# Kernel tuning notes

Hardware: AMD Instinct MI355X
Metric: run time of the kernel (lower is better)

## Reference

```python
import jax, jax.numpy as jnp
import numpy as np

B, S, D = 2, 2048, 2048
H, HD = 16, 128          # n_heads, head_dim
RD = 64                  # rope_head_dim
ND = HD - RD             # nope_head_dim = 64
KVR, QR = 512, 1024      # kv_lora_rank, q_lora_rank
BASE = 10000.0
NEG = -1e30


def _apply_rope(t):
    # t: [B, H, S, RD]; GPT-NeoX half-split rotation
    half = RD // 2
    seq = t.shape[2]
    inv_freq = 1.0 / (BASE ** (jnp.arange(half, dtype=jnp.float32) / half))
    ang = jnp.arange(seq, dtype=jnp.float32)[:, None] * inv_freq  # [S, half]
    cos, sin = jnp.cos(ang), jnp.sin(ang)
    t1, t2 = t[..., :half], t[..., half:]
    return jnp.concatenate([t1 * cos - t2 * sin, t1 * sin + t2 * cos], axis=-1)


def setup_inputs() -> dict:
    key = jax.random.key(0)
    ks = jax.random.split(key, 9)
    def w(k, shape):  # weights stored [in, out], so y = x @ W
        return jax.random.normal(k, shape, jnp.float32) * (shape[0] ** -0.5)
    return {
        "x": jax.random.normal(ks[0], (B, S, D), jnp.float32),
        "Wq_down": w(ks[1], (D, QR)),
        "Wq_up": w(ks[2], (QR, H * ND)),
        "Wq_rope": w(ks[3], (QR, H * RD)),
        "Wkv_down": w(ks[4], (D, KVR)),
        "Wk_up": w(ks[5], (KVR, H * ND)),
        "Wk_rope": w(ks[6], (D, H * RD)),
        "Wv_up": w(ks[7], (KVR, H * HD)),
        "Wo": w(ks[8], (H * HD, D)),
    }


def reference(x, Wq_down, Wq_up, Wq_rope, Wkv_down, Wk_up, Wk_rope, Wv_up, Wo):
    b, s, _ = x.shape
    # low-rank query path
    q_lat = x @ Wq_down                                            # [B,S,QR]
    q_nope = (q_lat @ Wq_up).reshape(b, s, H, ND).transpose(0, 2, 1, 3)
    q_pe = (q_lat @ Wq_rope).reshape(b, s, H, RD).transpose(0, 2, 1, 3)
    # low-rank KV path (decoupled rope key comes straight from x)
    kv_lat = x @ Wkv_down                                          # [B,S,KVR]
    k_nope = (kv_lat @ Wk_up).reshape(b, s, H, ND).transpose(0, 2, 1, 3)
    k_pe = (x @ Wk_rope).reshape(b, s, H, RD).transpose(0, 2, 1, 3)
    v = (kv_lat @ Wv_up).reshape(b, s, H, HD).transpose(0, 2, 1, 3)
    # decoupled RoPE on the PE branches only
    q_pe = _apply_rope(q_pe)
    k_pe = _apply_rope(k_pe)
    q = jnp.concatenate([q_nope, q_pe], axis=-1)                   # [B,H,S,HD]
    k = jnp.concatenate([k_nope, k_pe], axis=-1)                   # [B,H,S,HD]
    # causal SDPA (no mask/cache supplied -> is_causal=True)
    scale = HD ** -0.5
    scores = jnp.einsum("bhqd,bhkd->bhqk", q, k) * scale
    causal = jnp.tril(jnp.ones((s, s), dtype=bool))
    scores = jnp.where(causal, scores, NEG)
    attn = jax.nn.softmax(scores, axis=-1)
    out = jnp.einsum("bhqk,bhkd->bhqd", attn, v)
    out = out.transpose(0, 2, 1, 3).reshape(b, s, H * HD)
    return out @ Wo
```

## Files before the change

kernel.cpp:

```cpp
#include <hip/hip_runtime.h>
#include <hip/hip_bf16.h>

typedef unsigned short u16;
typedef short bf16x8 __attribute__((ext_vector_type(8)));
typedef float f32x4 __attribute__((ext_vector_type(4)));

static __device__ __forceinline__ u16 f2b(float f) {
  unsigned u = __float_as_uint(f);
  u += 0x7fffu + ((u >> 16) & 1u);
  return (u16)(u >> 16);
}
static __device__ __forceinline__ float b2f(u16 h) {
  return __uint_as_float(((unsigned)h) << 16);
}
static __device__ __forceinline__ f32x4 mfma16(bf16x8 a, bf16x8 b, f32x4 c) {
  return __builtin_amdgcn_mfma_f32_16x16x32_bf16(a, b, c, 0, 0, 0);
}
static __device__ __forceinline__ float fexp2(float x) {
  return __builtin_amdgcn_exp2f(x);
}

__device__ __align__(16) float g_rope[2048][64];

__global__ void rope_fill()
{
  int i = blockIdx.x * 256 + threadIdx.x;
  int s = i >> 5, j = i & 31;
  float invf = __expf(-(float)j * 0.28782313662425575f);
  float ang = (float)s * invf;
  g_rope[s][j] = cosf(ang);
  g_rope[s][32 + j] = sinf(ang);
}

__global__ void conv_f32_bf16(const float* __restrict__ src, u16* __restrict__ dst, int n4)
{
  int stride = gridDim.x * blockDim.x;
  for (int i = blockIdx.x * blockDim.x + threadIdx.x; i < n4; i += stride) {
    float4 v = ((const float4*)src)[i];
    ushort4 o;
    o.x = f2b(v.x); o.y = f2b(v.y); o.z = f2b(v.z); o.w = f2b(v.w);
    ((ushort4*)dst)[i] = o;
  }
}

__global__ void wtrans(const float* __restrict__ src, int K, int N,
                       u16* __restrict__ dst, int dld, int roff)
{
  __shared__ float tile[32][33];
  int n0 = blockIdx.x << 5, k0 = blockIdx.y << 5;
  int tx = threadIdx.x & 31, ty = threadIdx.x >> 5;
  #pragma unroll
  for (int p = 0; p < 4; ++p) {
    int kk = (p << 3) + ty;
    tile[kk][tx] = src[(size_t)(k0 + kk) * N + n0 + tx];
  }
  __syncthreads();
  #pragma unroll
  for (int p = 0; p < 4; ++p) {
    int nn = (p << 3) + ty;
    dst[(size_t)(roff + n0 + nn) * dld + k0 + tx] = f2b(tile[tx][nn]);
  }
}

__global__ __launch_bounds__(256, 2)
void gemm_bt(const u16* __restrict__ A, const u16* __restrict__ Bt,
             void* __restrict__ C, int K, int lda, int ldb, int ldc, int c_f32)
{
  __shared__ u16 As[128 * 64];
  __shared__ u16 Bs[128 * 64];
  const int t = threadIdx.x;
  const int lane = t & 63;
  const int m0 = blockIdx.y << 7, n0 = blockIdx.x << 7;
  const int w = t >> 6;
  const int wm = (w >> 1) << 6;
  const int wn = (w & 1) << 6;
  const int r15 = lane & 15, hi = lane >> 4;

  f32x4 acc[4][4];
  #pragma unroll
  for (int i = 0; i < 4; ++i)
    #pragma unroll
    for (int j = 0; j < 4; ++j)
      acc[i][j] = (f32x4){0.f, 0.f, 0.f, 0.f};

  for (int kt = 0; kt < K; kt += 64) {
    __syncthreads();
    #pragma unroll
    for (int p = 0; p < 4; ++p) {
      int g = (p << 8) + t;
      int row = g >> 3;
      int sl = (g & 7) ^ (row & 7);
      const u16* ga = A + (size_t)(m0 + row) * lda + kt + (sl << 3);
      __builtin_amdgcn_global_load_lds(
          (const __attribute__((address_space(1))) void*)ga,
          (__attribute__((address_space(3))) void*)((char*)As + g * 16), 16, 0, 0);
      const u16* gb = Bt + (size_t)(n0 + row) * ldb + kt + (sl << 3);
      __builtin_amdgcn_global_load_lds(
          (const __attribute__((address_space(1))) void*)gb,
          (__attribute__((address_space(3))) void*)((char*)Bs + g * 16), 16, 0, 0);
    }
    __syncthreads();
    #pragma unroll
    for (int kk = 0; kk < 2; ++kk) {
      int ks = (kk << 2) + hi;
      bf16x8 af[4], bfr[4];
      #pragma unroll
      for (int mi = 0; mi < 4; ++mi) {
        int row = wm + (mi << 4) + r15;
        af[mi] = *(const bf16x8*)((const char*)As + row * 128 + ((ks ^ (row & 7)) << 4));
      }
      #pragma unroll
      for (int ni = 0; ni < 4; ++ni) {
        int row = wn + (ni << 4) + r15;
        bfr[ni] = *(const bf16x8*)((const char*)Bs + row * 128 + ((ks ^ (row & 7)) << 4));
      }
      #pragma unroll
      for (int mi = 0; mi < 4; ++mi)
        #pragma unroll
        for (int ni = 0; ni < 4; ++ni)
          acc[mi][ni] = mfma16(af[mi], bfr[ni], acc[mi][ni]);
    }
  }

  if (c_f32) {
    float* Cf = (float*)C;
    #pragma unroll
    for (int mi = 0; mi < 4; ++mi)
      #pragma unroll
      for (int ni = 0; ni < 4; ++ni) {
        int row = m0 + wm + (mi << 4) + (hi << 2);
        int col = n0 + wn + (ni << 4) + r15;
        #pragma unroll
        for (int r = 0; r < 4; ++r)
          Cf[(size_t)(row + r) * ldc + col] = acc[mi][ni][r];
      }
  } else {
    u16* Cb = (u16*)C;
    #pragma unroll
    for (int mi = 0; mi < 4; ++mi)
      #pragma unroll
      for (int ni = 0; ni < 4; ++ni) {
        int row = m0 + wm + (mi << 4) + (hi << 2);
        int col = n0 + wn + (ni << 4) + r15;
        #pragma unroll
        for (int r = 0; r < 4; ++r)
          Cb[(size_t)(row + r) * ldc + col] = f2b(acc[mi][ni][r]);
      }
  }
}

__global__ void pack_q(const u16* __restrict__ qout, u16* __restrict__ Qb)
{
  int rid = (blockIdx.x << 2) + (threadIdx.x >> 6);
  int lane = threadIdx.x & 63;
  int s = rid & 2047, h = (rid >> 11) & 15;
  int b = rid >> 15;
  const u16* src = qout + (size_t)((b << 11) + s) * 2048;
  const float scale = 0.12751743f;
  float vn = b2f(src[(h << 6) + lane]) * scale;
  int j = lane & 31;
  float t1 = b2f(src[1024 + (h << 6) + j]);
  float t2 = b2f(src[1024 + (h << 6) + 32 + j]);
  float c = g_rope[s][j], sn = g_rope[s][32 + j];
  float vp = (lane < 32) ? (t1 * c - t2 * sn) : (t1 * sn + t2 * c);
  vp *= scale;
  u16* dst = Qb + (size_t)rid * 128;
  dst[lane] = f2b(vn);
  dst[64 + lane] = f2b(vp);
}

__global__ void pack_k(const u16* __restrict__ kvout, const u16* __restrict__ lat1,
                       u16* __restrict__ Kb)
{
  int rid = (blockIdx.x << 2) + (threadIdx.x >> 6);
  int lane = threadIdx.x & 63;
  int s = rid & 2047, h = (rid >> 11) & 15;
  int b = rid >> 15;
  size_t row = (size_t)((b << 11) + s);
  float vn = b2f(kvout[row * 3072 + (h << 6) + lane]);
  int j = lane & 31;
  float t1 = b2f(lat1[row * 2560 + 1536 + (h << 6) + j]);
  float t2 = b2f(lat1[row * 2560 + 1536 + (h << 6) + 32 + j]);
  float c = g_rope[s][j], sn = g_rope[s][32 + j];
  float vp = (lane < 32) ? (t1 * c - t2 * sn) : (t1 * sn + t2 * c);
  u16* dst = Kb + (size_t)rid * 128;
  dst[lane] = f2b(vn);
  dst[64 + lane] = f2b(vp);
}

__global__ void pack_vt(const u16* __restrict__ kvout, u16* __restrict__ Vt)
{
  __shared__ u16 tile[32][33];
  int bi = blockIdx.x;
  int dt = bi & 3, st = (bi >> 2) & 63, h = (bi >> 8) & 15, b = bi >> 12;
  int tx = threadIdx.x & 31, ty = threadIdx.x >> 5;
  #pragma unroll
  for (int p = 0; p < 4; ++p) {
    int s = (st << 5) + (p << 3) + ty;
    tile[(p << 3) + ty][tx] =
        kvout[(size_t)((b << 11) + s) * 3072 + 1024 + (h << 7) + (dt << 5) + tx];
  }
  __syncthreads();
  #pragma unroll
  for (int p = 0; p < 4; ++p) {
    int d = (dt << 5) + (p << 3) + ty;
    Vt[(size_t)(((b << 4) + h) * 128 + d) * 2048 + (st << 5) + tx] = tile[tx][(p << 3) + ty];
  }
}

__global__ __launch_bounds__(512, 4)
void attn_fwd(const u16* __restrict__ Qb, const u16* __restrict__ Kb,
              const u16* __restrict__ Vt, u16* __restrict__ AO)
{
  __shared__ __align__(16) u16 Kl[64 * 128];
  __shared__ __align__(16) u16 Vl[128 * 64];
  __shared__ __align__(16) u16 Pl[8][16 * 64];

  const int S = 2048;
  int g = (int)(blockIdx.x >> 5);
  int qtg = (g < 8) ? (15 - g) : (g - 8);
  int bh = blockIdx.x & 31;
  int b = bh >> 4, h = bh & 15;
  int t = threadIdx.x, lane = t & 63, w = t >> 6;
  int q0 = qtg << 7;
  int qw = q0 + (w << 4);
  int r15 = lane & 15, hi = lane >> 4;

  const u16* Qp = Qb + (size_t)bh * S * 128;
  const u16* Kp = Kb + (size_t)bh * S * 128;
  const u16* Vp = Vt + (size_t)bh * 128 * S;

  bf16x8 qf[4];
  #pragma unroll
  for (int kk = 0; kk < 4; ++kk)
    qf[kk] = *(const bf16x8*)(Qp + (size_t)(qw + r15) * 128 + kk * 32 + hi * 8);

  f32x4 o[8];
  #pragma unroll
  for (int i = 0; i < 8; ++i) o[i] = (f32x4){0.f, 0.f, 0.f, 0.f};
  float mrun = -1e30f, lrun = 0.f;

  int qme = qw + r15;
  u16* pw = Pl[w];

  int ntiles = (qtg << 1) + 2;
  for (int kt = 0; kt < ntiles; ++kt) {
    int kv0 = kt << 6;
    __syncthreads();
    #pragma unroll
    for (int p = 0; p < 2; ++p) {
      int gg = t + (p << 9);
      int rk = gg >> 4, ck = gg & 15, sk = ck ^ (rk & 15);
      const u16* ga = Kp + (size_t)(kv0 + rk) * 128 + (sk << 3);
      __builtin_amdgcn_global_load_lds(
          (const __attribute__((address_space(1))) void*)ga,
          (__attribute__((address_space(3))) void*)((char*)Kl + gg * 16), 16, 0, 0);
      int rv = gg >> 3, cv = gg & 7, sv = cv ^ (rv & 7);
      const u16* gv = Vp + (size_t)rv * S + kv0 + (sv << 3);
      __builtin_amdgcn_global_load_lds(
          (const __attribute__((address_space(1))) void*)gv,
          (__attribute__((address_space(3))) void*)((char*)Vl + gg * 16), 16, 0, 0);
    }
    __syncthreads();

    if (kv0 <= qw + 15) {
      f32x4 sc[4];
      __builtin_amdgcn_s_setprio(1);
      #pragma unroll
      for (int nt = 0; nt < 4; ++nt) {
        f32x4 a = (f32x4){0.f, 0.f, 0.f, 0.f};
        int row = (nt << 4) + r15;
        #pragma unroll
        for (int kk = 0; kk < 4; ++kk) {
          int ch = (kk << 2) + hi;
          bf16x8 kf = *(const bf16x8*)((const char*)Kl + row * 256 + ((ch ^ (row & 15)) << 4));
          a = mfma16(kf, qf[kk], a);
        }
        sc[nt] = a;
      }
      __builtin_amdgcn_s_setprio(0);

      if (kv0 + 63 > qw) {
        #pragma unroll
        for (int nt = 0; nt < 4; ++nt) {
          int kvb = kv0 + (nt << 4) + (hi << 2);
          #pragma unroll
          for (int r = 0; r < 4; ++r)
            sc[nt][r] = (kvb + r <= qme) ? sc[nt][r] : -1e30f;
        }
      }

      f32x4 mx = sc[0];
      #pragma unroll
      for (int nt = 1; nt < 4; ++nt) {
        mx[0] = fmaxf(mx[0], sc[nt][0]); mx[1] = fmaxf(mx[1], sc[nt][1]);
        mx[2] = fmaxf(mx[2], sc[nt][2]); mx[3] = fmaxf(mx[3], sc[nt][3]);
      }
      float mt = fmaxf(fmaxf(mx[0], mx[1]), fmaxf(mx[2], mx[3]));
      mt = fmaxf(mt, __shfl_xor(mt, 16, 64));
      mt = fmaxf(mt, __shfl_xor(mt, 32, 64));
      float mn = fmaxf(mrun, mt);
      float cr = fexp2(mrun - mn);
      float ps = 0.f;
      #pragma unroll
      for (int nt = 0; nt < 4; ++nt) {
        #pragma unroll
        for (int r = 0; r < 4; ++r) {
          float pv = fexp2(sc[nt][r] - mn);
          sc[nt][r] = pv;
          ps += pv;
        }
      }
      ps += __shfl_xor(ps, 16, 64);
      ps += __shfl_xor(ps, 32, 64);
      lrun = lrun * cr + ps;
      mrun = mn;

      #pragma unroll
      for (int dt = 0; dt < 8; ++dt) {
        f32x4 t4 = o[dt];
        t4[0] *= cr; t4[1] *= cr; t4[2] *= cr; t4[3] *= cr;
        o[dt] = t4;
      }

      #pragma unroll
      for (int nt = 0; nt < 4; ++nt) {
        ushort4 pk;
        pk.x = f2b(sc[nt][0]); pk.y = f2b(sc[nt][1]);
        pk.z = f2b(sc[nt][2]); pk.w = f2b(sc[nt][3]);
        int chunk = ((nt << 1) + (hi >> 1)) ^ (r15 & 7);
        *(ushort4*)((char*)pw + r15 * 128 + (chunk << 4) + ((hi & 1) << 3)) = pk;
      }

      bf16x8 pf[2];
      #pragma unroll
      for (int m = 0; m < 2; ++m) {
        int chunk = ((m << 2) + hi) ^ (r15 & 7);
        pf[m] = *(const bf16x8*)((const char*)pw + r15 * 128 + (chunk << 4));
      }
      __builtin_amdgcn_s_setprio(1);
      #pragma unroll
      for (int dt = 0; dt < 8; ++dt) {
        int vrow = (dt << 4) + r15;
        #pragma unroll
        for (int m = 0; m < 2; ++m) {
          int chv = (m << 2) + hi;
          bf16x8 vf = *(const bf16x8*)((const char*)Vl + vrow * 128 + ((chv ^ (vrow & 7)) << 4));
          o[dt] = mfma16(vf, pf[m], o[dt]);
        }
      }
      __builtin_amdgcn_s_setprio(0);
    }
  }

  float inv = 1.0f / lrun;
  size_t rowb = (size_t)(b * 2048 + qw + r15) * 2048 + h * 128 + (hi << 2);
  #pragma unroll
  for (int dt = 0; dt < 8; ++dt) {
    ushort4 ov;
    ov.x = f2b(o[dt][0] * inv); ov.y = f2b(o[dt][1] * inv);
    ov.z = f2b(o[dt][2] * inv); ov.w = f2b(o[dt][3] * inv);
    *(ushort4*)(AO + rowb + (dt << 4)) = ov;
  }
}

extern "C" void kernel_launch(void* const* d_in, const int* in_sizes, int n_in,
                              void* d_out, int out_size, void* d_ws, size_t ws_size,
                              hipStream_t stream)
{
  const float* x        = (const float*)d_in[0];
  const float* Wq_down  = (const float*)d_in[1];
  const float* Wq_up    = (const float*)d_in[2];
  const float* Wq_rope  = (const float*)d_in[3];
  const float* Wkv_down = (const float*)d_in[4];
  const float* Wk_up    = (const float*)d_in[5];
  const float* Wk_rope  = (const float*)d_in[6];
  const float* Wv_up    = (const float*)d_in[7];
  const float* Wo       = (const float*)d_in[8];

  char* ws = (char*)d_ws;
  u16* xb    = (u16*)(ws + 0);
  u16* W1t   = (u16*)(ws + 16777216);
  u16* W2t   = (u16*)(ws + 27262976);
  u16* W3t   = (u16*)(ws + 31457280);
  u16* Wot   = (u16*)(ws + 34603008);
  u16* lat1  = (u16*)(ws + 42991616);
  u16* qout  = (u16*)(ws + 63963136);
  u16* kvout = (u16*)(ws + 80740352);
  u16* Qb    = (u16*)(ws + 105906176);
  u16* Kb    = (u16*)(ws + 122683392);
  u16* Vtb   = (u16*)(ws + 139460608);
  u16* AO    = xb;
  if (ws_size < 156237824u) return;

  rope_fill<<<256, 256, 0, stream>>>();
  conv_f32_bf16<<<2048, 256, 0, stream>>>(x, xb, 2097152);

  wtrans<<<dim3(32, 64), 256, 0, stream>>>(Wq_down,  2048, 1024, W1t, 2048, 0);
  wtrans<<<dim3(16, 64), 256, 0, stream>>>(Wkv_down, 2048,  512, W1t, 2048, 1024);
  wtrans<<<dim3(32, 64), 256, 0, stream>>>(Wk_rope,  2048, 1024, W1t, 2048, 1536);
  wtrans<<<dim3(32, 32), 256, 0, stream>>>(Wq_up,    1024, 1024, W2t, 1024, 0);
  wtrans<<<dim3(32, 32), 256, 0, stream>>>(Wq_rope,  1024, 1024, W2t, 1024, 1024);
  wtrans<<<dim3(32, 16), 256, 0, stream>>>(Wk_up,     512, 1024, W3t,  512, 0);
  wtrans<<<dim3(64, 16), 256, 0, stream>>>(Wv_up,     512, 2048, W3t,  512, 1024);
  wtrans<<<dim3(64, 64), 256, 0, stream>>>(Wo,       2048, 2048, Wot, 2048, 0);

  gemm_bt<<<dim3(20, 32), 256, 0, stream>>>(xb, W1t, lat1, 2048, 2048, 2048, 2560, 0);
  gemm_bt<<<dim3(16, 32), 256, 0, stream>>>(lat1, W2t, qout, 1024, 2560, 1024, 2048, 0);
  gemm_bt<<<dim3(24, 32), 256, 0, stream>>>(lat1 + 1024, W3t, kvout, 512, 2560, 512, 3072, 0);

  pack_q<<<16384, 256, 0, stream>>>(qout, Qb);
  pack_k<<<16384, 256, 0, stream>>>(kvout, lat1, Kb);
  pack_vt<<<8192, 256, 0, stream>>>(kvout, Vtb);

  attn_fwd<<<512, 512, 0, stream>>>(Qb, Kb, Vtb, AO);

  gemm_bt<<<dim3(16, 32), 256, 0, stream>>>(AO, Wot, d_out, 2048, 2048, 2048, 2048, 1);

  (void)in_sizes; (void)n_in; (void)out_size;
}
```

Before: 389.5 us.

## Double-buffer LDS tiles in GEMM and attention K loads to overlap with compute

The GEMM kernel now keeps two LDS buffers for its A and B tiles. It issues the async global-to-LDS loads for the next K slice before computing on the current one, and uses one barrier per iteration. The attention kernel double-buffers its K tile and loads the V tile while the QK^T and softmax step runs, with a barrier placed before the PV product. The aim is to hide global load latency behind MFMA work. The extra LDS (64KB per attention block) can lower occupancy, and attention still needs two barriers per tile.

Result: slower. 436.5 us (+12.1%).

```diff
diff --git a/kernel.cpp b/kernel.cpp
--- a/kernel.cpp
+++ b/kernel.cpp
@@ -4,6 +4,10 @@
 typedef unsigned short u16;
 typedef short bf16x8 __attribute__((ext_vector_type(8)));
 typedef float f32x4 __attribute__((ext_vector_type(4)));
+
+#define GLDS16(gp, lp) __builtin_amdgcn_global_load_lds( \
+    (const __attribute__((address_space(1))) void*)(gp), \
+    (__attribute__((address_space(3))) void*)(lp), 16, 0, 0)
 
 static __device__ __forceinline__ u16 f2b(float f) {
   unsigned u = __float_as_uint(f);
@@ -66,8 +70,8 @@
 void gemm_bt(const u16* __restrict__ A, const u16* __restrict__ Bt,
              void* __restrict__ C, int K, int lda, int ldb, int ldc, int c_f32)
 {
-  __shared__ u16 As[128 * 64];
-  __shared__ u16 Bs[128 * 64];
+  __shared__ u16 As[2][128 * 64];
+  __shared__ u16 Bs[2][128 * 64];
   const int t = threadIdx.x;
   const int lane = t & 63;
   const int m0 = blockIdx.y << 7, n0 = blockIdx.x << 7;
@@ -83,23 +87,28 @@
     for (int j = 0; j < 4; ++j)
       acc[i][j] = (f32x4){0.f, 0.f, 0.f, 0.f};
 
-  for (int kt = 0; kt < K; kt += 64) {
-    __syncthreads();
+  auto STAGE = [&](int buf, int kt) {
     #pragma unroll
     for (int p = 0; p < 4; ++p) {
       int g = (p << 8) + t;
       int row = g >> 3;
       int sl = (g & 7) ^ (row & 7);
       const u16* ga = A + (size_t)(m0 + row) * lda + kt + (sl << 3);
-      __builtin_amdgcn_global_load_lds(
-          (const __attribute__((address_space(1))) void*)ga,
-          (__attribute__((address_space(3))) void*)((char*)As + g * 16), 16, 0, 0);
+      GLDS16(ga, (char*)As[buf] + g * 16);
       const u16* gb = Bt + (size_t)(n0 + row) * ldb + kt + (sl << 3);
-      __builtin_amdgcn_global_load_lds(
-          (const __attribute__((address_space(1))) void*)gb,
-          (__attribute__((address_space(3))) void*)((char*)Bs + g * 16), 16, 0, 0);
-    }
-    __syncthreads();
+      GLDS16(gb, (char*)Bs[buf] + g * 16);
+    }
+  };
+
+  const int nk = K >> 6;
+  STAGE(0, 0);
+  __syncthreads();
+
+  for (int ki = 0; ki < nk; ++ki) {
+    int kn = (ki + 1 < nk) ? ki + 1 : ki;
+    STAGE((ki + 1) & 1, kn << 6);
+    const char* Ab = (const char*)As[ki & 1];
+    const char* Bb = (const char*)Bs[ki & 1];
     #pragma unroll
     for (int kk = 0; kk < 2; ++kk) {
       int ks = (kk << 2) + hi;
@@ -107,12 +116,12 @@
       #pragma unroll
       for (int mi = 0; mi < 4; ++mi) {
         int row = wm + (mi << 4) + r15;
-        af[mi] = *(const bf16x8*)((const char*)As + row * 128 + ((ks ^ (row & 7)) << 4));
+        af[mi] = *(const bf16x8*)(Ab + row * 128 + ((ks ^ (row & 7)) << 4));
       }
       #pragma unroll
       for (int ni = 0; ni < 4; ++ni) {
         int row = wn + (ni << 4) + r15;
-        bfr[ni] = *(const bf16x8*)((const char*)Bs + row * 128 + ((ks ^ (row & 7)) << 4));
+        bfr[ni] = *(const bf16x8*)(Bb + row * 128 + ((ks ^ (row & 7)) << 4));
       }
       #pragma unroll
       for (int mi = 0; mi < 4; ++mi)
@@ -120,6 +129,7 @@
         for (int ni = 0; ni < 4; ++ni)
           acc[mi][ni] = mfma16(af[mi], bfr[ni], acc[mi][ni]);
     }
+    __syncthreads();
   }
 
   if (c_f32) {
@@ -212,7 +222,7 @@
 void attn_fwd(const u16* __restrict__ Qb, const u16* __restrict__ Kb,
               const u16* __restrict__ Vt, u16* __restrict__ AO)
 {
-  __shared__ __align__(16) u16 Kl[64 * 128];
+  __shared__ __align__(16) u16 Kl[2][64 * 128];
   __shared__ __align__(16) u16 Vl[128 * 64];
   __shared__ __align__(16) u16 Pl[8][16 * 64];
 
@@ -243,27 +253,39 @@
   int qme = qw + r15;
   u16* pw = Pl[w];
 
-  int ntiles = (qtg << 1) + 2;
-  for (int kt = 0; kt < ntiles; ++kt) {
-    int kv0 = kt << 6;
-    __syncthreads();
+  auto STAGE_K = [&](int buf, int kt) {
     #pragma unroll
     for (int p = 0; p < 2; ++p) {
       int gg = t + (p << 9);
       int rk = gg >> 4, ck = gg & 15, sk = ck ^ (rk & 15);
-      const u16* ga = Kp + (size_t)(kv0 + rk) * 128 + (sk << 3);
-      __builtin_amdgcn_global_load_lds(
-          (const __attribute__((address_space(1))) void*)ga,
-          (__attribute__((address_space(3))) void*)((char*)Kl + gg * 16), 16, 0, 0);
+      const u16* ga = Kp + (size_t)((kt << 6) + rk) * 128 + (sk << 3);
+      GLDS16(ga, (char*)Kl[buf] + gg * 16);
+    }
+  };
+  auto STAGE_V = [&](int kt) {
+    #pragma unroll
+    for (int p = 0; p < 2; ++p) {
+      int gg = t + (p << 9);
       int rv = gg >> 3, cv = gg & 7, sv = cv ^ (rv & 7);
-      const u16* gv = Vp + (size_t)rv * S + kv0 + (sv << 3);
-      __builtin_amdgcn_global_load_lds(
-          (const __attribute__((address_space(1))) void*)gv,
-          (__attribute__((address_space(3))) void*)((char*)Vl + gg * 16), 16, 0, 0);
-    }
-    __syncthreads();
-
-    if (kv0 <= qw + 15) {
+      const u16* gv = Vp + (size_t)rv * S + (kt << 6) + (sv << 3);
+      GLDS16(gv, (char*)Vl + gg * 16);
+    }
+  };
+
+  const int ntiles = (qtg << 1) + 2;
+  STAGE_K(0, 0);
+  __syncthreads();
+
+  for (int kt = 0; kt < ntiles; ++kt) {
+    int kv0 = kt << 6;
+    int ktn = (kt + 1 < ntiles) ? kt + 1 : kt;
+    STAGE_V(kt);
+    STAGE_K((kt + 1) & 1, ktn);
+
+    bool part = (kv0 <= qw + 15);
+    bf16x8 pf[2];
+    if (part) {
+      const char* Kcur = (const char*)Kl[kt & 1];
       f32x4 sc[4];
       __builtin_amdgcn_s_setprio(1);
       #pragma unroll
@@ -273,7 +295,7 @@
         #pragma unroll
         for (int kk = 0; kk < 4; ++kk) {
           int ch = (kk << 2) + hi;
-          bf16x8 kf = *(const bf16x8*)((const char*)Kl + row * 256 + ((ch ^ (row & 15)) << 4));
+          bf16x8 kf = *(const bf16x8*)(Kcur + row * 256 + ((ch ^ (row & 15)) << 4));
           a = mfma16(kf, qf[kk], a);
         }
         sc[nt] = a;
@@ -331,13 +353,16 @@
         int chunk = ((nt << 1) + (hi >> 1)) ^ (r15 & 7);
         *(ushort4*)((char*)pw + r15 * 128 + (chunk << 4) + ((hi & 1) << 3)) = pk;
       }
-
-      bf16x8 pf[2];
       #pragma unroll
       for (int m = 0; m < 2; ++m) {
         int chunk = ((m << 2) + hi) ^ (r15 & 7);
         pf[m] = *(const bf16x8*)((const char*)pw + r15 * 128 + (chunk << 4));
       }
+    }
+
+    __syncthreads();
+
+    if (part) {
       __builtin_amdgcn_s_setprio(1);
       #pragma unroll
       for (int dt = 0; dt < 8; ++dt) {
@@ -351,6 +376,8 @@
       }
       __builtin_amdgcn_s_setprio(0);
     }
+
+    __syncthreads();
   }
 
   float inv = 1.0f / lrun;
```
